# Kernel optimization log

Measured on AMD Instinct MI355X. Metric: run time of the kernel, lower is better.

Reference implementation:

```python
import jax, jax.numpy as jnp
import numpy as np

D_MODEL = 1024

def setup_inputs() -> dict:
    key = jax.random.key(0)
    ks = jax.random.split(key, 7)
    B, S, D = 4, 2048, D_MODEL
    scale = 1.0 / np.sqrt(D)
    x = jax.random.normal(ks[0], (B, S, D), dtype=jnp.float32)
    Wq = jax.random.normal(ks[1], (D, D), dtype=jnp.float32) * scale
    bq = jax.random.normal(ks[2], (D,), dtype=jnp.float32) * 0.02
    Wk = jax.random.normal(ks[3], (D, D), dtype=jnp.float32) * scale
    bk = jax.random.normal(ks[4], (D,), dtype=jnp.float32) * 0.02
    Wv = jax.random.normal(ks[5], (D, D), dtype=jnp.float32) * scale
    bv = jax.random.normal(ks[6], (D,), dtype=jnp.float32) * 0.02
    return {"x": x, "Wq": Wq, "bq": bq, "Wk": Wk, "bk": bk, "Wv": Wv, "bv": bv}

def reference(x, Wq, bq, Wk, bk, Wv, bv):
    # x: [B, S, D]
    B, S, D = x.shape
    q = jnp.einsum('bsd,de->bse', x, Wq) + bq
    k = jnp.einsum('bsd,de,->bse'.replace(',->', '->'), x, Wk) + bk
    v = jnp.einsum('bsd,de->bse', x, Wv) + bv
    # scores: [B, S, S], scaled by 1/sqrt(d_model) with additive causal mask
    scores = jnp.einsum('bqd,bkd->bqk', q, k) / jnp.sqrt(jnp.float32(D))
    causal = jnp.triu(jnp.full((S, S), -jnp.inf, dtype=scores.dtype), k=1)
    probs = jax.nn.softmax(scores + causal, axis=-1)
    return jnp.einsum('bqk,bkd->bqd', probs, v)
```

## Files before the change

kernel.cpp:

```cpp
#include <hip/hip_runtime.h>
#include <hip/hip_bf16.h>

#define S_LEN 2048
#define DM 1024
#define NB 4

typedef __attribute__((ext_vector_type(8))) short short8;
typedef __attribute__((ext_vector_type(4))) short short4v;
typedef __attribute__((ext_vector_type(4))) float floatx4;

__device__ inline short f2bf(float f) {
    union { float f; unsigned u; } v; v.f = f;
    unsigned r = 0x7fffu + ((v.u >> 16) & 1u);
    return (short)((v.u + r) >> 16);
}

__device__ inline void load16(const short* g, short* l) {
    __builtin_amdgcn_global_load_lds(
        (const __attribute__((address_space(1))) void*)g,
        (__attribute__((address_space(3))) void*)l,
        16, 0, 0);
}

__device__ inline void gemm_core128(const short* __restrict__ A,
                                    const short* __restrict__ Bt,
                                    int lda, int ldb, int kLen,
                                    int m0, int n0, floatx4 acc[4][4],
                                    short* As, short* Bs) {
    const int tid  = threadIdx.x;
    const int lane = tid & 63;
    const int wave = tid >> 6;
    const int wr   = (wave >> 1) * 64;
    const int wc   = (wave & 1) * 64;
    const int quad = lane >> 4;
    const int l16  = lane & 15;

    const int srow = tid >> 4;
    const int g    = (tid & 15) ^ srow;
    const short* gA0 = A  + (size_t)(m0 + srow) * lda + g * 8;
    const short* gB0 = Bt + (size_t)(n0 + srow) * ldb + g * 8;
    short* lA0 = &As[wave * 512];
    short* lB0 = &Bs[wave * 512];

    const short* fa[4]; const short* fb[4];
#pragma unroll
    for (int h = 0; h < 4; h++) {
        int sw = ((h * 4 + quad) ^ l16) * 8;
        fa[h] = &As[(wr + l16) * 128 + sw];
        fb[h] = &Bs[(wc + l16) * 128 + sw];
    }

    for (int k0 = 0; k0 < kLen; k0 += 128) {
#pragma unroll
        for (int c = 0; c < 8; c++) load16(gA0 + (size_t)c * 16 * lda, lA0 + c * 2048);
#pragma unroll
        for (int c = 0; c < 8; c++) load16(gB0 + (size_t)c * 16 * ldb, lB0 + c * 2048);
        gA0 += 128; gB0 += 128;
        __syncthreads();

#pragma unroll
        for (int h = 0; h < 4; h++) {
            short8 af[4], bf[4];
#pragma unroll
            for (int t = 0; t < 4; t++) af[t] = *(const short8*)(fa[h] + t * 2048);
#pragma unroll
            for (int t = 0; t < 4; t++) bf[t] = *(const short8*)(fb[h] + t * 2048);
#pragma unroll
            for (int mt = 0; mt < 4; mt++)
#pragma unroll
                for (int nt = 0; nt < 4; nt++)
                    acc[mt][nt] = __builtin_amdgcn_mfma_f32_16x16x32_bf16(
                        af[mt], bf[nt], acc[mt][nt], 0, 0, 0);
        }
        __syncthreads();
    }
}

__global__ void prep(const float* __restrict__ x,
                     const float* __restrict__ Wq, const float* __restrict__ Wk,
                     const float* __restrict__ Wv,
                     short* __restrict__ xb, short* __restrict__ Wt) {
    __shared__ float t[64][65];
    int bid = blockIdx.x, tid = threadIdx.x;
    if (bid < 768) {
        int w = bid >> 8, tl = bid & 255;
        const float* W = (w == 0) ? Wq : (w == 1) ? Wk : Wv;
        short* out = Wt + (size_t)w * DM * DM;
        int bx = (tl & 15) * 64;
        int by = (tl >> 4) * 64;
        int tx = tid & 63, ty = tid >> 6;
        for (int r = ty; r < 64; r += 4)
            t[r][tx] = W[(size_t)(by + r) * DM + bx + tx];
        __syncthreads();
        for (int r = ty; r < 64; r += 4)
            out[(size_t)(bx + r) * DM + by + tx] = f2bf(t[tx][r]);
    } else {
        int i = (bid - 768) * 256 + tid;
        float4 v = ((const float4*)x)[i];
        short4v o;
        o.x = f2bf(v.x); o.y = f2bf(v.y); o.z = f2bf(v.z); o.w = f2bf(v.w);
        ((short4v*)xb)[i] = o;
    }
}

__global__ __launch_bounds__(256, 2)
void qkv_fused(const short* __restrict__ xb, const short* __restrict__ Wt,
               const float* __restrict__ bq, const float* __restrict__ bk,
               const float* __restrict__ bv,
               short* __restrict__ Qb, short* __restrict__ Kb,
               short* __restrict__ Vtb) {
    __shared__ short As[8192];
    __shared__ short Bs[3 * 8192];
    int n0 = blockIdx.x * 128;
    int m0 = blockIdx.y * 128;

    const int tid  = threadIdx.x;
    const int lane = tid & 63;
    const int wave = tid >> 6;
    const int wr   = (wave >> 1) * 64;
    const int wc   = (wave & 1) * 64;
    const int quad = lane >> 4;
    const int l16  = lane & 15;

    floatx4 acc[3][4][4];
#pragma unroll
    for (int w = 0; w < 3; w++)
#pragma unroll
        for (int i = 0; i < 4; i++)
#pragma unroll
            for (int j = 0; j < 4; j++) acc[w][i][j] = (floatx4){0.f, 0.f, 0.f, 0.f};

    const short* gA[4]; const short* gW[4];
    short* lA[4]; short* lB[4];
#pragma unroll
    for (int c = 0; c < 4; c++) {
        int idx = c * 256 + tid;
        int row = idx >> 3;
        int g = (idx & 7) ^ (row & 7);
        gA[c] = xb + (size_t)(m0 + row) * DM + g * 8;
        gW[c] = Wt + (size_t)(n0 + row) * DM + g * 8;
        int lbase = (c * 256 + wave * 64) * 8;
        lA[c] = &As[lbase];
        lB[c] = &Bs[lbase];
    }

    const short* fa[2]; const short* fb[2];
#pragma unroll
    for (int h = 0; h < 2; h++) {
        int sw = ((h * 4 + quad) ^ (l16 & 7)) * 8;
        fa[h] = &As[(wr + l16) * 64 + sw];
        fb[h] = &Bs[(wc + l16) * 64 + sw];
    }

    for (int k0 = 0; k0 < DM; k0 += 64) {
#pragma unroll
        for (int c = 0; c < 4; c++) load16(gA[c], lA[c]);
#pragma unroll
        for (int w = 0; w < 3; w++)
#pragma unroll
            for (int c = 0; c < 4; c++)
                load16(gW[c] + (size_t)w * DM * DM, lB[c] + w * 8192);
#pragma unroll
        for (int c = 0; c < 4; c++) { gA[c] += 64; gW[c] += 64; }
        __syncthreads();

#pragma unroll
        for (int h = 0; h < 2; h++) {
            short8 af[4];
#pragma unroll
            for (int t = 0; t < 4; t++) af[t] = *(const short8*)(fa[h] + t * 1024);
#pragma unroll
            for (int w = 0; w < 3; w++) {
                short8 bf[4];
#pragma unroll
                for (int t = 0; t < 4; t++)
                    bf[t] = *(const short8*)(fb[h] + w * 8192 + t * 1024);
#pragma unroll
                for (int mt = 0; mt < 4; mt++)
#pragma unroll
                    for (int nt = 0; nt < 4; nt++)
                        acc[w][mt][nt] = __builtin_amdgcn_mfma_f32_16x16x32_bf16(
                            af[mt], bf[nt], acc[w][mt][nt], 0, 0, 0);
            }
        }
        __syncthreads();
    }

#pragma unroll
    for (int w = 0; w < 2; w++) {
        short* out = w ? Kb : Qb;
        const float* bias = w ? bk : bq;
        float scale = w ? 1.0f : 0.03125f;
#pragma unroll
        for (int mt = 0; mt < 4; mt++)
#pragma unroll
            for (int nt = 0; nt < 4; nt++) {
                int col = n0 + wc + nt * 16 + l16;
                float bv_ = bias[col];
#pragma unroll
                for (int r = 0; r < 4; r++) {
                    int row = m0 + wr + mt * 16 + quad * 4 + r;
                    out[(size_t)row * DM + col] = f2bf((acc[w][mt][nt][r] + bv_) * scale);
                }
            }
    }

    {
        int b = m0 >> 11;
        int sbase = (m0 & 2047) + wr;
        float bvv[4];
#pragma unroll
        for (int nt = 0; nt < 4; nt++) bvv[nt] = bv[n0 + wc + nt * 16 + l16];
        short* buf = (wave & 1) ? Bs : As;
        short* vt = Vtb + ((size_t)b * DM + n0 + wc) * S_LEN;
#pragma unroll
        for (int p = 0; p < 2; p++) {
            __syncthreads();
            if ((wave >> 1) == p) {
#pragma unroll
                for (int mt = 0; mt < 4; mt++)
#pragma unroll
                    for (int nt = 0; nt < 4; nt++) {
                        int c = nt * 16 + l16;
                        short4v pk;
                        pk.x = f2bf(acc[2][mt][nt][0] + bvv[nt]);
                        pk.y = f2bf(acc[2][mt][nt][1] + bvv[nt]);
                        pk.z = f2bf(acc[2][mt][nt][2] + bvv[nt]);
                        pk.w = f2bf(acc[2][mt][nt][3] + bvv[nt]);
                        *(short4v*)&buf[c * 72 + mt * 16 + quad * 4] = pk;
                    }
                asm volatile("s_waitcnt lgkmcnt(0)" ::: "memory");
#pragma unroll
                for (int ps = 0; ps < 8; ps++) {
                    int dl = ps * 8 + (lane >> 3);
                    int sl = (lane & 7) * 8;
                    short8 row = *(short8*)&buf[dl * 72 + sl];
                    *(short8*)(vt + (size_t)dl * S_LEN + sbase + sl) = row;
                }
            }
        }
    }
}

__global__ __launch_bounds__(256, 2)
void score_gemm(const short* __restrict__ Qb, const short* __restrict__ Kb,
                short* __restrict__ P, float* __restrict__ denom) {
    __shared__ short As[16384];
    __shared__ short Bs[16384];
    int bid = blockIdx.x;
    int xcd = bid & 7;
    int w   = bid >> 3;
    int b   = w / 17;
    int s   = w % 17;
    int it  = (s <= xcd) ? xcd : 15 - xcd;
    int jt  = (s <= xcd) ? s : s - xcd - 1;
    int n0 = jt * 128, m0 = it * 128;
    const short* A  = Qb + (size_t)b * S_LEN * DM;
    const short* Bt = Kb + (size_t)b * S_LEN * DM;

    floatx4 acc[4][4];
#pragma unroll
    for (int i = 0; i < 4; i++)
#pragma unroll
        for (int j = 0; j < 4; j++) acc[i][j] = (floatx4){0.f, 0.f, 0.f, 0.f};

    gemm_core128(A, Bt, DM, DM, DM, m0, n0, acc, As, Bs);

    short* out = P + (size_t)b * S_LEN * S_LEN;
    float* dsum = denom + (size_t)b * S_LEN;
    const int lane = threadIdx.x & 63, wave = threadIdx.x >> 6;
    const int wr = (wave >> 1) * 64, wc = (wave & 1) * 64;
    const int quad = lane >> 4, l16 = lane & 15;
    const bool diag = (jt == it);
#pragma unroll
    for (int mt = 0; mt < 4; mt++) {
#pragma unroll
        for (int r = 0; r < 4; r++) {
            int row = m0 + wr + mt * 16 + quad * 4 + r;
            float psum = 0.f;
#pragma unroll
            for (int nt = 0; nt < 4; nt++) {
                int col = n0 + wc + nt * 16 + l16;
                float e = __expf(acc[mt][nt][r]);
                if (diag && col > row) e = 0.f;
                out[(size_t)row * S_LEN + col] = f2bf(e);
                psum += e;
            }
#pragma unroll
            for (int off = 8; off > 0; off >>= 1)
                psum += __shfl_down(psum, off, 16);
            if (l16 == 0) atomicAdd(&dsum[row], psum);
        }
    }
}

__global__ __launch_bounds__(256, 2)
void pv_gemm(const short* __restrict__ P, const short* __restrict__ Vtb,
             const float* __restrict__ denom, float* __restrict__ O) {
    __shared__ short As[16384];
    __shared__ short Bs[16384];
    int bid  = blockIdx.x;
    int xcd  = bid & 7;
    int wi   = bid >> 3;
    int b    = xcd >> 1;
    int dgrp = xcd & 1;
    int half = wi >> 5;
    int r    = (wi >> 2) & 7;
    int dl   = wi & 3;
    int it   = half ? r : 15 - r;
    int n0   = (dgrp * 4 + dl) * 128;
    int m0   = it * 128;
    int kLen = (it + 1) * 128;
    const short* A  = P   + (size_t)b * S_LEN * S_LEN;
    const short* Bt = Vtb + (size_t)b * DM * S_LEN;

    floatx4 acc[4][4];
#pragma unroll
    for (int i = 0; i < 4; i++)
#pragma unroll
        for (int j = 0; j < 4; j++) acc[i][j] = (floatx4){0.f, 0.f, 0.f, 0.f};

    gemm_core128(A, Bt, S_LEN, S_LEN, kLen, m0, n0, acc, As, Bs);

    float* out = O + (size_t)b * S_LEN * DM;
    const float* dsum = denom + (size_t)b * S_LEN;
    const int lane = threadIdx.x & 63, wave = threadIdx.x >> 6;
    const int wr = (wave >> 1) * 64, wc = (wave & 1) * 64;
    const int quad = lane >> 4, l16 = lane & 15;
#pragma unroll
    for (int mt = 0; mt < 4; mt++) {
#pragma unroll
        for (int r2 = 0; r2 < 4; r2++) {
            int row = m0 + wr + mt * 16 + quad * 4 + r2;
            float inv = 1.0f / dsum[row];
#pragma unroll
            for (int nt = 0; nt < 4; nt++) {
                int col = n0 + wc + nt * 16 + l16;
                out[(size_t)row * DM + col] = acc[mt][nt][r2] * inv;
            }
        }
    }
}

extern "C" void kernel_launch(void* const* d_in, const int* in_sizes, int n_in,
                              void* d_out, int out_size, void* d_ws, size_t ws_size,
                              hipStream_t stream) {
    const float* x  = (const float*)d_in[0];
    const float* Wq = (const float*)d_in[1];
    const float* bq = (const float*)d_in[2];
    const float* Wk = (const float*)d_in[3];
    const float* bk = (const float*)d_in[4];
    const float* Wv = (const float*)d_in[5];
    const float* bv = (const float*)d_in[6];
    float* out = (float*)d_out;

    char* ws = (char*)d_ws;
    const size_t MB = 1u << 20;
    short* xb    = (short*)(ws + 0);
    short* Wt    = (short*)(ws + 16 * MB);
    short* Qb    = (short*)(ws + 22 * MB);
    short* Kb    = (short*)(ws + 38 * MB);
    short* Vtb   = (short*)(ws + 54 * MB);
    short* P     = (short*)(ws + 70 * MB);
    float* denom = (float*)(ws + 102 * MB);

    hipMemsetAsync(denom, 0, (size_t)NB * S_LEN * sizeof(float), stream);
    prep<<<dim3(8960), dim3(256), 0, stream>>>(x, Wq, Wk, Wv, xb, Wt);
    qkv_fused<<<dim3(8, 64), dim3(256), 0, stream>>>(xb, Wt, bq, bk, bv, Qb, Kb, Vtb);
    score_gemm<<<dim3(544), dim3(256), 0, stream>>>(Qb, Kb, P, denom);
    pv_gemm<<<dim3(512), dim3(256), 0, stream>>>(P, Vtb, denom, out);
}
```

Before: 216.9 us.

## Double-buffer LDS tiles in GEMM core with K-step of 64

Replaces the single-buffered 128-wide K loop with a double-buffered 64-wide K loop. The async global-to-LDS loads for the next K slice are issued before computing on the current buffer, so memory latency can overlap with MFMA work. Each iteration now has one barrier instead of two. LDS footprint stays the same, but the loop runs twice as many iterations with half the MFMA work per sync, and the swizzle changes to fit the 64-wide rows.

```diff
diff --git a/kernel.cpp b/kernel.cpp
--- a/kernel.cpp
+++ b/kernel.cpp
@@ -22,9 +22,9 @@
         16, 0, 0);
 }
 
-__device__ inline void gemm_core128(const short* __restrict__ A,
+__device__ inline void gemm_core_db(const short* __restrict__ A,
                                     const short* __restrict__ Bt,
-                                    int lda, int ldb, int kLen,
+                                    int lda, int ldb, int kIters,
                                     int m0, int n0, floatx4 acc[4][4],
                                     short* As, short* Bs) {
     const int tid  = threadIdx.x;
@@ -35,36 +35,49 @@
     const int quad = lane >> 4;
     const int l16  = lane & 15;
 
-    const int srow = tid >> 4;
-    const int g    = (tid & 15) ^ srow;
-    const short* gA0 = A  + (size_t)(m0 + srow) * lda + g * 8;
-    const short* gB0 = Bt + (size_t)(n0 + srow) * ldb + g * 8;
-    short* lA0 = &As[wave * 512];
-    short* lB0 = &Bs[wave * 512];
-
-    const short* fa[4]; const short* fb[4];
-#pragma unroll
-    for (int h = 0; h < 4; h++) {
-        int sw = ((h * 4 + quad) ^ l16) * 8;
-        fa[h] = &As[(wr + l16) * 128 + sw];
-        fb[h] = &Bs[(wc + l16) * 128 + sw];
-    }
-
-    for (int k0 = 0; k0 < kLen; k0 += 128) {
-#pragma unroll
-        for (int c = 0; c < 8; c++) load16(gA0 + (size_t)c * 16 * lda, lA0 + c * 2048);
-#pragma unroll
-        for (int c = 0; c < 8; c++) load16(gB0 + (size_t)c * 16 * ldb, lB0 + c * 2048);
-        gA0 += 128; gB0 += 128;
-        __syncthreads();
-
-#pragma unroll
-        for (int h = 0; h < 4; h++) {
+    const short* gA[4]; const short* gB[4];
+#pragma unroll
+    for (int c = 0; c < 4; c++) {
+        int idx = c * 256 + tid;
+        int row = idx >> 3;
+        int g = (idx & 7) ^ (row & 7);
+        gA[c] = A  + (size_t)(m0 + row) * lda + g * 8;
+        gB[c] = Bt + (size_t)(n0 + row) * ldb + g * 8;
+    }
+    const int lo = wave * 512;
+
+    const short* fa[2]; const short* fb[2];
+#pragma unroll
+    for (int h = 0; h < 2; h++) {
+        int sw = ((h * 4 + quad) ^ (l16 & 7)) * 8;
+        fa[h] = &As[(wr + l16) * 64 + sw];
+        fb[h] = &Bs[(wc + l16) * 64 + sw];
+    }
+
+#pragma unroll
+    for (int c = 0; c < 4; c++) load16(gA[c], As + lo + c * 2048);
+#pragma unroll
+    for (int c = 0; c < 4; c++) load16(gB[c], Bs + lo + c * 2048);
+    __syncthreads();
+
+    int buf = 0;
+    for (int k = 0; k < kIters; k++) {
+        if (k + 1 < kIters) {
+            const int nb = (buf ^ 1) * 8192;
+            const int ko = (k + 1) * 64;
+#pragma unroll
+            for (int c = 0; c < 4; c++) load16(gA[c] + ko, As + nb + lo + c * 2048);
+#pragma unroll
+            for (int c = 0; c < 4; c++) load16(gB[c] + ko, Bs + nb + lo + c * 2048);
+        }
+        const int bo = buf * 8192;
+#pragma unroll
+        for (int h = 0; h < 2; h++) {
             short8 af[4], bf[4];
 #pragma unroll
-            for (int t = 0; t < 4; t++) af[t] = *(const short8*)(fa[h] + t * 2048);
-#pragma unroll
-            for (int t = 0; t < 4; t++) bf[t] = *(const short8*)(fb[h] + t * 2048);
+            for (int t = 0; t < 4; t++) af[t] = *(const short8*)(fa[h] + bo + t * 1024);
+#pragma unroll
+            for (int t = 0; t < 4; t++) bf[t] = *(const short8*)(fb[h] + bo + t * 1024);
 #pragma unroll
             for (int mt = 0; mt < 4; mt++)
 #pragma unroll
@@ -73,6 +86,7 @@
                         af[mt], bf[nt], acc[mt][nt], 0, 0, 0);
         }
         __syncthreads();
+        buf ^= 1;
     }
 }
 
@@ -245,8 +259,8 @@
 __global__ __launch_bounds__(256, 2)
 void score_gemm(const short* __restrict__ Qb, const short* __restrict__ Kb,
                 short* __restrict__ P, float* __restrict__ denom) {
-    __shared__ short As[16384];
-    __shared__ short Bs[16384];
+    __shared__ short As[2 * 8192];
+    __shared__ short Bs[2 * 8192];
     int bid = blockIdx.x;
     int xcd = bid & 7;
     int w   = bid >> 3;
@@ -264,7 +278,7 @@
 #pragma unroll
         for (int j = 0; j < 4; j++) acc[i][j] = (floatx4){0.f, 0.f, 0.f, 0.f};
 
-    gemm_core128(A, Bt, DM, DM, DM, m0, n0, acc, As, Bs);
+    gemm_core_db(A, Bt, DM, DM, DM / 64, m0, n0, acc, As, Bs);
 
     short* out = P + (size_t)b * S_LEN * S_LEN;
     float* dsum = denom + (size_t)b * S_LEN;
@@ -297,8 +311,8 @@
 __global__ __launch_bounds__(256, 2)
 void pv_gemm(const short* __restrict__ P, const short* __restrict__ Vtb,
              const float* __restrict__ denom, float* __restrict__ O) {
-    __shared__ short As[16384];
-    __shared__ short Bs[16384];
+    __shared__ short As[2 * 8192];
+    __shared__ short Bs[2 * 8192];
     int bid  = blockIdx.x;
     int xcd  = bid & 7;
     int wi   = bid >> 3;
@@ -310,7 +324,7 @@
     int it   = half ? r : 15 - r;
     int n0   = (dgrp * 4 + dl) * 128;
     int m0   = it * 128;
-    int kLen = (it + 1) * 128;
+    int kIters = (it + 1) * 2;
     const short* A  = P   + (size_t)b * S_LEN * S_LEN;
     const short* Bt = Vtb + (size_t)b * DM * S_LEN;
 
@@ -320,7 +334,7 @@
 #pragma unroll
         for (int j = 0; j < 4; j++) acc[i][j] = (floatx4){0.f, 0.f, 0.f, 0.f};
 
-    gemm_core128(A, Bt, S_LEN, S_LEN, kLen, m0, n0, acc, As, Bs);
+    gemm_core_db(A, Bt, S_LEN, S_LEN, kIters, m0, n0, acc, As, Bs);
 
     float* out = O + (size_t)b * S_LEN * DM;
     const float* dsum = denom + (size_t)b * S_LEN;
```

Result: slower. 234.3 us (+8.0%).

## Widen score GEMM tiles to 128x256 with causal-aware tile mapping

Applied to the files above, without the earlier changes.

Rewrites score_gemm to compute 128x256 output tiles (each wave 64x128) with its own inline single-buffered K loop instead of the shared 128x128 gemm_core. The grid drops from 544 to 288 blocks, with a new XCD-aware mapping of lower-triangular tile pairs. This raises MFMA work per LDS load and cuts the number of blocks. In exchange it doubles the accumulator registers and computes some fully masked columns in diagonal tiles. It also loses any pipelining gemm_core128 had, and fewer blocks may underfill the 256 CUs.

```diff
diff --git a/kernel.cpp b/kernel.cpp
--- a/kernel.cpp
+++ b/kernel.cpp
@@ -245,33 +245,79 @@
 __global__ __launch_bounds__(256, 2)
 void score_gemm(const short* __restrict__ Qb, const short* __restrict__ Kb,
                 short* __restrict__ P, float* __restrict__ denom) {
-    __shared__ short As[16384];
-    __shared__ short Bs[16384];
-    int bid = blockIdx.x;
-    int xcd = bid & 7;
-    int w   = bid >> 3;
-    int b   = w / 17;
-    int s   = w % 17;
-    int it  = (s <= xcd) ? xcd : 15 - xcd;
-    int jt  = (s <= xcd) ? s : s - xcd - 1;
-    int n0 = jt * 128, m0 = it * 128;
+    __shared__ short As[128 * 64];
+    __shared__ short Bs[256 * 64];
+
+    const int bid = blockIdx.x;
+    const int xcd = bid & 7;
+    const int w   = bid >> 3;
+    const int b   = w / 9;
+    const int s   = w % 9;
+    const int cx  = (xcd + 2) >> 1;
+    const int it  = (s < cx) ? xcd : 15 - xcd;
+    const int jt2 = (s < cx) ? s : s - cx;
+    const int m0  = it * 128;
+    const int n0  = jt2 * 256;
+
     const short* A  = Qb + (size_t)b * S_LEN * DM;
     const short* Bt = Kb + (size_t)b * S_LEN * DM;
 
-    floatx4 acc[4][4];
+    const int tid  = threadIdx.x;
+    const int lane = tid & 63;
+    const int wave = tid >> 6;
+    const int wr   = (wave >> 1) * 64;
+    const int wc   = (wave & 1) * 128;
+    const int quad = lane >> 4;
+    const int l16  = lane & 15;
+
+    floatx4 acc[4][8];
 #pragma unroll
     for (int i = 0; i < 4; i++)
 #pragma unroll
-        for (int j = 0; j < 4; j++) acc[i][j] = (floatx4){0.f, 0.f, 0.f, 0.f};
-
-    gemm_core128(A, Bt, DM, DM, DM, m0, n0, acc, As, Bs);
+        for (int j = 0; j < 8; j++) acc[i][j] = (floatx4){0.f, 0.f, 0.f, 0.f};
+
+    const int g = (tid & 7) ^ ((tid >> 3) & 7);
+    const short* gA0 = A  + (size_t)(m0 + (tid >> 3)) * DM + g * 8;
+    const short* gB0 = Bt + (size_t)(n0 + (tid >> 3)) * DM + g * 8;
+    short* lA0 = &As[wave * 512];
+    short* lB0 = &Bs[wave * 512];
+
+    const short* fa[2]; const short* fb[2];
+#pragma unroll
+    for (int h = 0; h < 2; h++) {
+        int sw = ((h * 4 + quad) ^ (l16 & 7)) * 8;
+        fa[h] = &As[(wr + l16) * 64 + sw];
+        fb[h] = &Bs[(wc + l16) * 64 + sw];
+    }
+
+    for (int k0 = 0; k0 < DM; k0 += 64) {
+#pragma unroll
+        for (int c = 0; c < 4; c++) load16(gA0 + (size_t)c * 32 * DM, lA0 + c * 2048);
+#pragma unroll
+        for (int c = 0; c < 8; c++) load16(gB0 + (size_t)c * 32 * DM, lB0 + c * 2048);
+        gA0 += 64; gB0 += 64;
+        __syncthreads();
+
+#pragma unroll
+        for (int h = 0; h < 2; h++) {
+            short8 af[4];
+#pragma unroll
+            for (int t = 0; t < 4; t++) af[t] = *(const short8*)(fa[h] + t * 1024);
+            short8 bf[8];
+#pragma unroll
+            for (int t = 0; t < 8; t++) bf[t] = *(const short8*)(fb[h] + t * 1024);
+#pragma unroll
+            for (int mt = 0; mt < 4; mt++)
+#pragma unroll
+                for (int nt = 0; nt < 8; nt++)
+                    acc[mt][nt] = __builtin_amdgcn_mfma_f32_16x16x32_bf16(
+                        af[mt], bf[nt], acc[mt][nt], 0, 0, 0);
+        }
+        __syncthreads();
+    }
 
     short* out = P + (size_t)b * S_LEN * S_LEN;
     float* dsum = denom + (size_t)b * S_LEN;
-    const int lane = threadIdx.x & 63, wave = threadIdx.x >> 6;
-    const int wr = (wave >> 1) * 64, wc = (wave & 1) * 64;
-    const int quad = lane >> 4, l16 = lane & 15;
-    const bool diag = (jt == it);
 #pragma unroll
     for (int mt = 0; mt < 4; mt++) {
 #pragma unroll
@@ -279,10 +325,9 @@
             int row = m0 + wr + mt * 16 + quad * 4 + r;
             float psum = 0.f;
 #pragma unroll
-            for (int nt = 0; nt < 4; nt++) {
+            for (int nt = 0; nt < 8; nt++) {
                 int col = n0 + wc + nt * 16 + l16;
-                float e = __expf(acc[mt][nt][r]);
-                if (diag && col > row) e = 0.f;
+                float e = (col <= row) ? __expf(acc[mt][nt][r]) : 0.f;
                 out[(size_t)row * S_LEN + col] = f2bf(e);
                 psum += e;
             }
@@ -367,6 +412,6 @@
     hipMemsetAsync(denom, 0, (size_t)NB * S_LEN * sizeof(float), stream);
     prep<<<dim3(8960), dim3(256), 0, stream>>>(x, Wq, Wk, Wv, xb, Wt);
     qkv_fused<<<dim3(8, 64), dim3(256), 0, stream>>>(xb, Wt, bq, bk, bv, Qb, Kb, Vtb);
-    score_gemm<<<dim3(544), dim3(256), 0, stream>>>(Qb, Kb, P, denom);
+    score_gemm<<<dim3(288), dim3(256), 0, stream>>>(Qb, Kb, P, denom);
     pv_gemm<<<dim3(512), dim3(256), 0, stream>>>(P, Vtb, denom, out);
 }
```

Result: faster. 207.7 us (-4.3%).
